# Kernel tuning notes

Measured on AMD Instinct MI355X. Metric: run time of the kernel, lower is better.

Reference implementation:

```python
import jax
import jax.numpy as jnp
import numpy as np

TIME_DIVISION = 2
FILL_DIST = 50000.0  # sentinel initial distance, as in the torch module


def setup_inputs() -> dict:
    key = jax.random.key(0)
    k1, k2 = jax.random.split(key)
    B, T, H, W, C = 4, 16, 28, 28, 35
    TT = T // TIME_DIVISION
    x = jax.random.normal(k1, (B, T, H, W, C), dtype=jnp.float32)
    init_ = jax.random.randint(k2, (B * TIME_DIVISION,), 0, TT * H * W, dtype=jnp.int64)
    return {"x": x, "init_": init_, "k": 256}


def _pairwise_dist(xf):
    # xf: (Bt, N, C) -> (Bt, N, N) euclidean distances (torch.cdist p=2)
    sq = jnp.sum(xf * xf, axis=-1)                      # (Bt, N)
    gram = jnp.einsum('bnc,bmc->bnm', xf, xf)           # (Bt, N, N)
    d2 = jnp.maximum(sq[:, :, None] + sq[:, None, :] - 2.0 * gram, 0.0)
    return jnp.sqrt(d2)


def reference(x, init_, k):
    B, T, H, W, C = x.shape
    TT = T // TIME_DIVISION
    N = TT * H * W                 # points per time segment
    Bt = B * TIME_DIVISION
    k_ = k // TIME_DIVISION

    xf = x.reshape(Bt, N, C)
    cdist = _pairwise_dist(xf)
    # set diagonal to -1 (self-distance excluded from argmax)
    diag = jnp.arange(N)
    cdist = cdist.at[:, diag, diag].set(-1.0)

    b_idx = jnp.arange(Bt)
    farthest0 = jnp.remainder(init_, N)
    distance0 = jnp.full((Bt, N), FILL_DIST, dtype=x.dtype)

    def step(carry, _):
        distance, farthest = carry
        dist = cdist[b_idx, farthest]                   # (Bt, N) gather rows
        distance = jnp.minimum(dist, distance)
        farthest = jnp.argmax(distance, axis=-1)
        return (distance, farthest), farthest

    _, rest = jax.lax.scan(step, (distance0, farthest0), None, length=k_ - 1)
    sampling_index = jnp.concatenate([farthest0[None], rest], axis=0).T  # (Bt, k_)

    # add per-time-segment index offsets, flatten to (B, td*k_)
    offsets = (jnp.arange(TIME_DIVISION) * (TT * H * W))[None, :, None]
    sampling_index = sampling_index.reshape(B, TIME_DIVISION, k_) + offsets
    sampling_index = sampling_index.reshape(B, TIME_DIVISION * k_)

    # gather feature channels (first C-3; last 3 are positional encodings)
    xflat = x.reshape(B, T * H * W, C)
    patches = xflat[jnp.arange(B)[:, None], sampling_index][:, :, : C - 3]
    return patches, sampling_index
```

## Files before the change

### kernel.cpp

```cpp
#include <hip/hip_runtime.h>


#define NPTS 6272
#define CDIM 35
#define BT   8
#define KSEL 128
#define THW  12544
#define BPS  16
#define PPB  392
#define BLK  256
#define NB   (BT * BPS)
#define TAILN (PPB - BLK)

__device__ __forceinline__ unsigned long long key_of(float v, int j) {
  unsigned int u = __float_as_uint(v);
  u = (u & 0x80000000u) ? ~u : (u | 0x80000000u);
  return ((unsigned long long)u << 32) | (unsigned int)(NPTS - j);
}
__device__ __forceinline__ unsigned long long kmax(unsigned long long a,
                                                   unsigned long long b) {
  return a > b ? a : b;
}

template <int CTRL, int RMASK, bool BC>
__device__ __forceinline__ unsigned long long dpp_kmax(unsigned long long k) {
  unsigned int lo = (unsigned int)k, hi = (unsigned int)(k >> 32);
  unsigned int tlo = (unsigned int)__builtin_amdgcn_update_dpp(0, (int)lo, CTRL, RMASK, 0xF, BC);
  unsigned int thi = (unsigned int)__builtin_amdgcn_update_dpp(0, (int)hi, CTRL, RMASK, 0xF, BC);
  unsigned long long t = ((unsigned long long)thi << 32) | tlo;
  return kmax(k, t);
}

__device__ __forceinline__ unsigned long long wave_kmax64(unsigned long long k) {
  k = dpp_kmax<0x111, 0xF, true >(k);
  k = dpp_kmax<0x112, 0xF, true >(k);
  k = dpp_kmax<0x114, 0xF, true >(k);
  k = dpp_kmax<0x118, 0xF, true >(k);
  k = dpp_kmax<0x142, 0xA, false>(k);
  k = dpp_kmax<0x143, 0xC, false>(k);
  unsigned int rlo = (unsigned int)__builtin_amdgcn_readlane((int)(unsigned int)k, 63);
  unsigned int rhi = (unsigned int)__builtin_amdgcn_readlane((int)(k >> 32), 63);
  return ((unsigned long long)rhi << 32) | rlo;
}

__device__ __forceinline__ unsigned long long row16_kmax(unsigned long long k) {
  k = dpp_kmax<0x111, 0xF, true>(k);
  k = dpp_kmax<0x112, 0xF, true>(k);
  k = dpp_kmax<0x114, 0xF, true>(k);
  k = dpp_kmax<0x118, 0xF, true>(k);
  unsigned int rlo = (unsigned int)__builtin_amdgcn_readlane((int)(unsigned int)k, 15);
  unsigned int rhi = (unsigned int)__builtin_amdgcn_readlane((int)(k >> 32), 15);
  return ((unsigned long long)rhi << 32) | rlo;
}

__device__ __forceinline__ unsigned long long poll_slot(const unsigned long long* p) {
  unsigned int klo = 0u, khi = 0u;
  unsigned int a0, b0, a1, b1, a2, b2, t;
  asm volatile(
      "global_load_dword %[a0], %[ad], off sc0 sc1\n\t"
      "global_load_dword %[b0], %[ad], off offset:4 sc0 sc1\n\t"
      "global_load_dword %[a1], %[ad], off sc0 sc1\n\t"
      "global_load_dword %[b1], %[ad], off offset:4 sc0 sc1\n\t"
      "global_load_dword %[a2], %[ad], off sc0 sc1\n\t"
      "global_load_dword %[b2], %[ad], off offset:4 sc0 sc1\n\t"
      "1:\n\t"
      "s_waitcnt vmcnt(4)\n\t"
      "v_max_u32 %[klo], %[klo], %[a0]\n\t"
      "v_max_u32 %[khi], %[khi], %[b0]\n\t"
      "global_load_dword %[a0], %[ad], off sc0 sc1\n\t"
      "global_load_dword %[b0], %[ad], off offset:4 sc0 sc1\n\t"
      "v_min_u32 %[t], %[klo], %[khi]\n\t"
      "v_cmp_eq_u32 vcc, 0, %[t]\n\t"
      "s_cbranch_vccz 9f\n\t"
      "s_waitcnt vmcnt(4)\n\t"
      "v_max_u32 %[klo], %[klo], %[a1]\n\t"
      "v_max_u32 %[khi], %[khi], %[b1]\n\t"
      "global_load_dword %[a1], %[ad], off sc0 sc1\n\t"
      "global_load_dword %[b1], %[ad], off offset:4 sc0 sc1\n\t"
      "v_min_u32 %[t], %[klo], %[khi]\n\t"
      "v_cmp_eq_u32 vcc, 0, %[t]\n\t"
      "s_cbranch_vccz 9f\n\t"
      "s_waitcnt vmcnt(4)\n\t"
      "v_max_u32 %[klo], %[klo], %[a2]\n\t"
      "v_max_u32 %[khi], %[khi], %[b2]\n\t"
      "global_load_dword %[a2], %[ad], off sc0 sc1\n\t"
      "global_load_dword %[b2], %[ad], off offset:4 sc0 sc1\n\t"
      "v_min_u32 %[t], %[klo], %[khi]\n\t"
      "v_cmp_eq_u32 vcc, 0, %[t]\n\t"
      "s_cbranch_vccnz 1b\n\t"
      "9:\n\t"
      "s_waitcnt vmcnt(0)"
      : [klo] "+v"(klo), [khi] "+v"(khi),
        [a0] "=&v"(a0), [b0] "=&v"(b0), [a1] "=&v"(a1), [b1] "=&v"(b1),
        [a2] "=&v"(a2), [b2] "=&v"(b2), [t] "=&v"(t)
      : [ad] "v"(p)
      : "vcc", "memory");
  return ((unsigned long long)khi << 32) | klo;
}

__global__ __attribute__((amdgpu_waves_per_eu(1, 1))) __launch_bounds__(BLK)
void fps_kernel(const float* __restrict__ x,
                const int* __restrict__ init_,
                int* __restrict__ out_idx,
                unsigned long long* __restrict__ slots) {
  __shared__ unsigned long long wk[4];
  __shared__ int far_s;

  const int bid  = (int)blockIdx.x;
  const int b    = bid & 7;
  const int sub  = bid >> 3;
  const int tid  = (int)threadIdx.x;
  const int lane = tid & 63;
  const int wid  = tid >> 6;
  const int j0   = sub * PPB;
  const float* xg = x + (size_t)b * NPTS * CDIM;
  unsigned long long* seg = slots + (size_t)b * KSEL * BPS;

  float xr0[CDIM], xr1[CDIM];
  float sqr0, sqr1, df0, df1;
  {
    const float* src0 = xg + (size_t)(j0 + tid) * CDIM;
    float acc = 0.0f;
    {
#pragma clang fp contract(off)
#pragma unroll
      for (int c = 0; c < CDIM; ++c) { float v = src0[c]; xr0[c] = v; acc = acc + v * v; }
    }
    sqr0 = acc; df0 = 50000.0f;
    sqr1 = 0.0f; df1 = 50000.0f;
#pragma unroll
    for (int c = 0; c < CDIM; ++c) xr1[c] = 0.0f;
    if (tid < TAILN) {
      const float* src1 = xg + (size_t)(j0 + BLK + tid) * CDIM;
      float acc1 = 0.0f;
      {
#pragma clang fp contract(off)
#pragma unroll
        for (int c = 0; c < CDIM; ++c) { float v = src1[c]; xr1[c] = v; acc1 = acc1 + v * v; }
      }
      sqr1 = acc1;
    }
#pragma unroll
    for (int c = 0; c < CDIM; ++c) {
      asm volatile("" : "+v"(xr0[c]));
      asm volatile("" : "+v"(xr1[c]));
    }
    asm volatile("" : "+v"(sqr0));
    asm volatile("" : "+v"(sqr1));
  }

  int far;
  { int f = init_[b] % NPTS; if (f < 0) f += NPTS; far = f; }
  if (sub == 0 && tid == 0) out_idx[b * KSEL] = far;

  for (int step = 1; step < KSEL; ++step) {
    const int fu = __builtin_amdgcn_readfirstlane(far);
    const float* fx = xg + (size_t)fu * CDIM;
    float xf[CDIM];
#pragma unroll
    for (int c = 0; c < CDIM; ++c) xf[c] = fx[c];

    float sqf;
    {
#pragma clang fp contract(off)
      float a = 0.0f;
#pragma unroll
      for (int c = 0; c < CDIM; ++c) { float t = xf[c]; a = a + t * t; }
      sqf = a;
    }

    unsigned long long bk;
    {
      float dot = 0.0f;
#pragma unroll
      for (int c = 0; c < CDIM; ++c)
        dot = __builtin_fmaf(xf[c], xr0[c], dot);
      float d2;
      {
#pragma clang fp contract(off)
        d2 = (sqf + sqr0) - 2.0f * dot;
      }
      d2 = fmaxf(d2, 0.0f);
      float d = __fsqrt_rn(d2);
      const int j = j0 + tid;
      d = (j == far) ? -1.0f : d;
      float nd = fminf(d, df0);
      df0 = nd;
      bk = key_of(nd, j);
    }
    if (tid < TAILN) {
      float dot = 0.0f;
#pragma unroll
      for (int c = 0; c < CDIM; ++c)
        dot = __builtin_fmaf(xf[c], xr1[c], dot);
      float d2;
      {
#pragma clang fp contract(off)
        d2 = (sqf + sqr1) - 2.0f * dot;
      }
      d2 = fmaxf(d2, 0.0f);
      float d = __fsqrt_rn(d2);
      const int j = j0 + BLK + tid;
      d = (j == far) ? -1.0f : d;
      float nd = fminf(d, df1);
      df1 = nd;
      bk = kmax(bk, key_of(nd, j));
    }

    bk = wave_kmax64(bk);
    if (lane == 0) wk[wid] = bk;
    __syncthreads();

    if (tid < BPS) {
      if (tid == 0) {
        unsigned long long m = kmax(kmax(wk[0], wk[1]), kmax(wk[2], wk[3]));
        __hip_atomic_store(&seg[step * BPS + sub], m,
                           __ATOMIC_RELAXED, __HIP_MEMORY_SCOPE_AGENT);
      }
      asm volatile("" ::: "memory");
      unsigned long long k = poll_slot(&seg[step * BPS + tid]);
      k = row16_kmax(k);
      if (tid == 0) {
        int f = NPTS - (int)(unsigned int)(k & 0xFFFFFFFFull);
        far_s = f;
        if (sub == 0) out_idx[b * KSEL + step] = f;
      }
    }
    __syncthreads();
    far = far_s;
  }
}

__global__ __launch_bounds__(256) void gather_kernel(const float* __restrict__ x,
                                                     const int* __restrict__ out_idx,
                                                     float* __restrict__ patches,
                                                     float* __restrict__ sidx) {
  const int b = (int)blockIdx.x;
  const int m = (int)threadIdx.x;
  const int td = m >> 7;
  const int i  = m & 127;
  const int li = out_idx[(b * 2 + td) * KSEL + i];
  const int gi = li + td * NPTS;
  sidx[b * 256 + m] = (float)gi;
  const float* src = x + ((size_t)b * THW + gi) * CDIM;
  float* dst = patches + ((size_t)b * 256 + m) * 32;
#pragma unroll
  for (int c = 0; c < 32; ++c) dst[c] = src[c];
}

extern "C" void kernel_launch(void* const* d_in, const int* in_sizes, int n_in,
                              void* d_out, int out_size, void* d_ws, size_t ws_size,
                              hipStream_t stream) {
  const float* x    = (const float*)d_in[0];
  const int*   init = (const int*)d_in[1];
  (void)in_sizes; (void)n_in; (void)out_size; (void)ws_size;

  unsigned long long* slots = (unsigned long long*)d_ws;
  const size_t slots_bytes = (size_t)BT * KSEL * BPS * sizeof(unsigned long long);
  int* idx = (int*)((char*)d_ws + slots_bytes);

  float* patches = (float*)d_out;
  float* sidx    = patches + (size_t)4 * 256 * 32;

  hipMemsetAsync(d_ws, 0, slots_bytes, stream);

  void* kargs[] = { (void*)&x, (void*)&init, (void*)&idx, (void*)&slots };
  hipLaunchCooperativeKernel((const void*)fps_kernel, dim3(NB), dim3(BLK),
                             kargs, 0, stream);

  hipLaunchKernelGGL(gather_kernel, dim3(4), dim3(256), 0, stream,
                     x, idx, patches, sidx);
}
```

Measured before the change: 225.3 us.

## Poll L2-cached probe slots for cross-block argmax and fuse gather into FPS kernel

Each block now writes its partial argmax key both to an LLC-coherent slot and to a plain-stored probe array. Other blocks mostly poll the probe with L2-level loads plus short sleeps, and fall back periodically to the system-coherent slot. This aims to cut the latency of the per-step inter-block exchange. The separate gather kernel is removed: block 0 of each segment writes the sampled index and patch row every step, and a start barrier makes sure the probe zeroing is done before use. The risks are L2 visibility across XCDs (the probe may never update, so the fallback path carries correctness) and more memset traffic.

```diff
diff --git a/kernel.cpp b/kernel.cpp
--- a/kernel.cpp
+++ b/kernel.cpp
@@ -21,6 +21,13 @@
                                                    unsigned long long b) {
   return a > b ? a : b;
 }
+__device__ __forceinline__ unsigned long long merge64(unsigned long long a,
+                                                      unsigned long long t) {
+  unsigned int lo = (unsigned int)a > (unsigned int)t ? (unsigned int)a : (unsigned int)t;
+  unsigned int ah = (unsigned int)(a >> 32), th = (unsigned int)(t >> 32);
+  unsigned int hi = ah > th ? ah : th;
+  return ((unsigned long long)hi << 32) | lo;
+}
 
 template <int CTRL, int RMASK, bool BC>
 __device__ __forceinline__ unsigned long long dpp_kmax(unsigned long long k) {
@@ -30,7 +37,6 @@
   unsigned long long t = ((unsigned long long)thi << 32) | tlo;
   return kmax(k, t);
 }
-
 __device__ __forceinline__ unsigned long long wave_kmax64(unsigned long long k) {
   k = dpp_kmax<0x111, 0xF, true >(k);
   k = dpp_kmax<0x112, 0xF, true >(k);
@@ -42,7 +48,6 @@
   unsigned int rhi = (unsigned int)__builtin_amdgcn_readlane((int)(k >> 32), 63);
   return ((unsigned long long)rhi << 32) | rlo;
 }
-
 __device__ __forceinline__ unsigned long long row16_kmax(unsigned long long k) {
   k = dpp_kmax<0x111, 0xF, true>(k);
   k = dpp_kmax<0x112, 0xF, true>(k);
@@ -53,56 +58,29 @@
   return ((unsigned long long)rhi << 32) | rlo;
 }
 
-__device__ __forceinline__ unsigned long long poll_slot(const unsigned long long* p) {
-  unsigned int klo = 0u, khi = 0u;
-  unsigned int a0, b0, a1, b1, a2, b2, t;
-  asm volatile(
-      "global_load_dword %[a0], %[ad], off sc0 sc1\n\t"
-      "global_load_dword %[b0], %[ad], off offset:4 sc0 sc1\n\t"
-      "global_load_dword %[a1], %[ad], off sc0 sc1\n\t"
-      "global_load_dword %[b1], %[ad], off offset:4 sc0 sc1\n\t"
-      "global_load_dword %[a2], %[ad], off sc0 sc1\n\t"
-      "global_load_dword %[b2], %[ad], off offset:4 sc0 sc1\n\t"
-      "1:\n\t"
-      "s_waitcnt vmcnt(4)\n\t"
-      "v_max_u32 %[klo], %[klo], %[a0]\n\t"
-      "v_max_u32 %[khi], %[khi], %[b0]\n\t"
-      "global_load_dword %[a0], %[ad], off sc0 sc1\n\t"
-      "global_load_dword %[b0], %[ad], off offset:4 sc0 sc1\n\t"
-      "v_min_u32 %[t], %[klo], %[khi]\n\t"
-      "v_cmp_eq_u32 vcc, 0, %[t]\n\t"
-      "s_cbranch_vccz 9f\n\t"
-      "s_waitcnt vmcnt(4)\n\t"
-      "v_max_u32 %[klo], %[klo], %[a1]\n\t"
-      "v_max_u32 %[khi], %[khi], %[b1]\n\t"
-      "global_load_dword %[a1], %[ad], off sc0 sc1\n\t"
-      "global_load_dword %[b1], %[ad], off offset:4 sc0 sc1\n\t"
-      "v_min_u32 %[t], %[klo], %[khi]\n\t"
-      "v_cmp_eq_u32 vcc, 0, %[t]\n\t"
-      "s_cbranch_vccz 9f\n\t"
-      "s_waitcnt vmcnt(4)\n\t"
-      "v_max_u32 %[klo], %[klo], %[a2]\n\t"
-      "v_max_u32 %[khi], %[khi], %[b2]\n\t"
-      "global_load_dword %[a2], %[ad], off sc0 sc1\n\t"
-      "global_load_dword %[b2], %[ad], off offset:4 sc0 sc1\n\t"
-      "v_min_u32 %[t], %[klo], %[khi]\n\t"
-      "v_cmp_eq_u32 vcc, 0, %[t]\n\t"
-      "s_cbranch_vccnz 1b\n\t"
-      "9:\n\t"
-      "s_waitcnt vmcnt(0)"
-      : [klo] "+v"(klo), [khi] "+v"(khi),
-        [a0] "=&v"(a0), [b0] "=&v"(b0), [a1] "=&v"(a1), [b1] "=&v"(b1),
-        [a2] "=&v"(a2), [b2] "=&v"(b2), [t] "=&v"(t)
-      : [ad] "v"(p)
-      : "vcc", "memory");
-  return ((unsigned long long)khi << 32) | klo;
+__device__ __forceinline__ unsigned long long load_l2(const unsigned long long* p) {
+  unsigned long long r;
+  asm volatile("global_load_dwordx2 %0, %1, off sc0\n\ts_waitcnt vmcnt(0)"
+               : "=&v"(r) : "v"(p) : "memory");
+  return r;
+}
+__device__ __forceinline__ unsigned long long load_llc(const unsigned long long* p) {
+  unsigned long long r;
+  asm volatile("global_load_dwordx2 %0, %1, off sc0 sc1\n\ts_waitcnt vmcnt(0)"
+               : "=&v"(r) : "v"(p) : "memory");
+  return r;
+}
+__device__ __forceinline__ void store_plain(unsigned long long* p, unsigned long long v) {
+  asm volatile("global_store_dwordx2 %0, %1, off" :: "v"(p), "v"(v) : "memory");
 }
 
 __global__ __attribute__((amdgpu_waves_per_eu(1, 1))) __launch_bounds__(BLK)
 void fps_kernel(const float* __restrict__ x,
                 const int* __restrict__ init_,
-                int* __restrict__ out_idx,
-                unsigned long long* __restrict__ slots) {
+                float* __restrict__ patches,
+                float* __restrict__ sidx,
+                unsigned long long* __restrict__ slots,
+                unsigned long long* __restrict__ probe) {
   __shared__ unsigned long long wk[4];
   __shared__ int far_s;
 
@@ -113,8 +91,13 @@
   const int lane = tid & 63;
   const int wid  = tid >> 6;
   const int j0   = sub * PPB;
+  const int td   = b & 1;
   const float* xg = x + (size_t)b * NPTS * CDIM;
   unsigned long long* seg = slots + (size_t)b * KSEL * BPS;
+  unsigned long long* prb = probe + (size_t)b * KSEL * BPS;
+
+  if (tid >= 1 && tid < KSEL)
+    store_plain(&prb[tid * BPS + sub], 0ull);
 
   float xr0[CDIM], xr1[CDIM];
   float sqr0, sqr1, df0, df1;
@@ -149,9 +132,21 @@
     asm volatile("" : "+v"(sqr1));
   }
 
+  asm volatile("s_waitcnt vmcnt(0)" ::: "memory");
+  if (tid == 0)
+    __hip_atomic_store(&seg[sub], 1ull, __ATOMIC_RELAXED, __HIP_MEMORY_SCOPE_AGENT);
+  if (tid < BPS) {
+    while (__hip_atomic_load(&seg[tid], __ATOMIC_RELAXED,
+                             __HIP_MEMORY_SCOPE_AGENT) == 0ull) {}
+  }
+  __syncthreads();
+
   int far;
   { int f = init_[b] % NPTS; if (f < 0) f += NPTS; far = f; }
-  if (sub == 0 && tid == 0) out_idx[b * KSEL] = far;
+  if (sub == 0) {
+    if (tid == 0) sidx[b * KSEL] = (float)(far + td * NPTS);
+    if (tid < 32) patches[(size_t)(b * KSEL) * 32 + tid] = xg[(size_t)far * CDIM + tid];
+  }
 
   for (int step = 1; step < KSEL; ++step) {
     const int fu = __builtin_amdgcn_readfirstlane(far);
@@ -214,38 +209,37 @@
     if (tid < BPS) {
       if (tid == 0) {
         unsigned long long m = kmax(kmax(wk[0], wk[1]), kmax(wk[2], wk[3]));
+        store_plain(&prb[step * BPS + sub], m);
         __hip_atomic_store(&seg[step * BPS + sub], m,
                            __ATOMIC_RELAXED, __HIP_MEMORY_SCOPE_AGENT);
       }
       asm volatile("" ::: "memory");
-      unsigned long long k = poll_slot(&seg[step * BPS + tid]);
+      unsigned long long k = 0ull;
+      const unsigned long long* pp = &prb[step * BPS + tid];
+      const unsigned long long* sp = &seg[step * BPS + tid];
+      while (__any(k == 0ull)) {
+#pragma unroll
+        for (int q = 0; q < 3; ++q) {
+          if (__any(k == 0ull)) {
+            if (k == 0ull) k = merge64(k, load_l2(pp));
+            __builtin_amdgcn_s_sleep(1);
+          }
+        }
+        if (k == 0ull) k = merge64(k, load_llc(sp));
+      }
       k = row16_kmax(k);
-      if (tid == 0) {
-        int f = NPTS - (int)(unsigned int)(k & 0xFFFFFFFFull);
-        far_s = f;
-        if (sub == 0) out_idx[b * KSEL + step] = f;
-      }
+      if (tid == 0)
+        far_s = NPTS - (int)(unsigned int)(k & 0xFFFFFFFFull);
     }
     __syncthreads();
     far = far_s;
-  }
-}
-
-__global__ __launch_bounds__(256) void gather_kernel(const float* __restrict__ x,
-                                                     const int* __restrict__ out_idx,
-                                                     float* __restrict__ patches,
-                                                     float* __restrict__ sidx) {
-  const int b = (int)blockIdx.x;
-  const int m = (int)threadIdx.x;
-  const int td = m >> 7;
-  const int i  = m & 127;
-  const int li = out_idx[(b * 2 + td) * KSEL + i];
-  const int gi = li + td * NPTS;
-  sidx[b * 256 + m] = (float)gi;
-  const float* src = x + ((size_t)b * THW + gi) * CDIM;
-  float* dst = patches + ((size_t)b * 256 + m) * 32;
-#pragma unroll
-  for (int c = 0; c < 32; ++c) dst[c] = src[c];
+
+    if (sub == 0) {
+      if (tid == 0) sidx[b * KSEL + step] = (float)(far + td * NPTS);
+      if (tid < 32) patches[(size_t)(b * KSEL + step) * 32 + tid] =
+                        xg[(size_t)far * CDIM + tid];
+    }
+  }
 }
 
 extern "C" void kernel_launch(void* const* d_in, const int* in_sizes, int n_in,
@@ -255,19 +249,17 @@
   const int*   init = (const int*)d_in[1];
   (void)in_sizes; (void)n_in; (void)out_size; (void)ws_size;
 
+  const size_t arr = (size_t)BT * KSEL * BPS * sizeof(unsigned long long);
   unsigned long long* slots = (unsigned long long*)d_ws;
-  const size_t slots_bytes = (size_t)BT * KSEL * BPS * sizeof(unsigned long long);
-  int* idx = (int*)((char*)d_ws + slots_bytes);
+  unsigned long long* probe = (unsigned long long*)((char*)d_ws + arr);
 
   float* patches = (float*)d_out;
   float* sidx    = patches + (size_t)4 * 256 * 32;
 
-  hipMemsetAsync(d_ws, 0, slots_bytes, stream);
-
-  void* kargs[] = { (void*)&x, (void*)&init, (void*)&idx, (void*)&slots };
+  hipMemsetAsync(d_ws, 0, 2 * arr, stream);
+
+  void* kargs[] = { (void*)&x, (void*)&init, (void*)&patches, (void*)&sidx,
+                    (void*)&slots, (void*)&probe };
   hipLaunchCooperativeKernel((const void*)fps_kernel, dim3(NB), dim3(BLK),
                              kargs, 0, stream);
-
-  hipLaunchKernelGGL(gather_kernel, dim3(4), dim3(256), 0, stream,
-                     x, idx, patches, sidx);
-}
+}
```

After: 218.5 us. -3.1%, faster.
